# Performance work log

Measured on AMD Instinct MI355X. Metric: run time of the kernel, lower is better.

## Reference

```python
import jax, jax.numpy as jnp
import numpy as np

N_NODES = 100000
HIDDEN = 64
N_EDGES = 1600000


def _sage_conv(x, edge_index, Wl, Wr, b):
    # PyG SAGEConv (mean aggr): out_i = W_l @ mean_{j->i} x_j + W_r @ x_i + b
    src, dst = edge_index[0], edge_index[1]
    msg = x[src]                                      # [E, H] gather
    agg = jax.ops.segment_sum(msg, dst, num_segments=N_NODES)  # [N, H]
    deg = jax.ops.segment_sum(jnp.ones((msg.shape[0],), x.dtype), dst,
                              num_segments=N_NODES)
    agg = agg / jnp.maximum(deg, 1.0)[:, None]
    return agg @ Wl.T + x @ Wr.T + b


def setup_inputs() -> dict:
    key = jax.random.key(0)
    ks = jax.random.split(key, 8)
    s = 1.0 / np.sqrt(HIDDEN)
    return {
        "emb": jax.random.normal(ks[0], (N_NODES, HIDDEN), jnp.float32),
        "Wl1": jax.random.normal(ks[1], (HIDDEN, HIDDEN), jnp.float32) * s,
        "Wr1": jax.random.normal(ks[2], (HIDDEN, HIDDEN), jnp.float32) * s,
        "b1": jnp.zeros((HIDDEN,), jnp.float32),
        "Wl2": jax.random.normal(ks[3], (HIDDEN, HIDDEN), jnp.float32) * s,
        "Wr2": jax.random.normal(ks[4], (HIDDEN, HIDDEN), jnp.float32) * s,
        "b2": jnp.zeros((HIDDEN,), jnp.float32),
        "node_id": jnp.arange(N_NODES, dtype=jnp.int64 if jax.config.jax_enable_x64 else jnp.int32),
        "edge_index": jax.random.randint(ks[5], (2, N_EDGES), 0, N_NODES),
    }


def reference(emb, Wl1, Wr1, b1, Wl2, Wr2, b2, node_id, edge_index):
    # Embedding lookup
    x = emb[node_id]                                   # [N, H]
    # GNN: relu(conv1) -> conv2
    x = jax.nn.relu(_sage_conv(x, edge_index, Wl1, Wr1, b1))
    x = _sage_conv(x, edge_index, Wl2, Wr2, b2)
    # Classifier: per-edge dot product of endpoint features
    ef1 = x[edge_index[0]]                             # [E, H]
    ef2 = x[edge_index[1]]                             # [E, H]
    return (ef1 * ef2).sum(axis=-1)                    # [E]
```

## Files before the change

### kernel.cpp

```cpp
#include <hip/hip_runtime.h>

#define N_NODES 100000
#define HID 64
#define N_EDGES 1600000
#define NB 391
#define NBP 392
#define NHB 256
#define C_EPB 6400
#define GATHER_BLOCKS 6250

typedef __attribute__((ext_vector_type(8))) short bf16x8;
typedef __attribute__((ext_vector_type(4))) float f32x4;

__device__ __forceinline__ unsigned short f2bf(float f) {
    unsigned u = __float_as_uint(f);
    u = (u + 0x7FFFu + ((u >> 16) & 1u)) >> 16;
    return (unsigned short)u;
}
__device__ __forceinline__ float bf2f(unsigned short h) {
    return __uint_as_float(((unsigned)h) << 16);
}
__device__ __forceinline__ float bflo(unsigned w) { return __uint_as_float(w << 16); }
__device__ __forceinline__ float bfhi(unsigned w) { return __uint_as_float(w & 0xFFFF0000u); }

__global__ void gather_hist_kernel(const float* __restrict__ emb,
                                   const int* __restrict__ nid,
                                   unsigned short* __restrict__ xh,
                                   const int* __restrict__ dst,
                                   int* __restrict__ bhist_part) {
    if (blockIdx.x < GATHER_BLOCKS) {
        int i = blockIdx.x * blockDim.x + threadIdx.x;
        const int total = N_NODES * (HID / 4);
        if (i >= total) return;
        int row = i >> 4;
        int c   = i & 15;
        int s   = nid[row];
        float4 v = reinterpret_cast<const float4*>(emb)[(size_t)s * 16 + c];
        uint2 p;
        p.x = (unsigned)f2bf(v.x) | ((unsigned)f2bf(v.y) << 16);
        p.y = (unsigned)f2bf(v.z) | ((unsigned)f2bf(v.w) << 16);
        reinterpret_cast<uint2*>(xh)[(size_t)row * 16 + c] = p;
        return;
    }
    __shared__ int h[NB];
    for (int i = threadIdx.x; i < NB; i += blockDim.x) h[i] = 0;
    __syncthreads();
    int hb = blockIdx.x - GATHER_BLOCKS;
    const int nt = NHB * 256;
    const int4* d4 = (const int4*)dst;
    for (int q = hb * blockDim.x + threadIdx.x; q < N_EDGES / 4; q += nt) {
        int4 v = d4[q];
        atomicAdd(&h[v.x >> 8], 1);
        atomicAdd(&h[v.y >> 8], 1);
        atomicAdd(&h[v.z >> 8], 1);
        atomicAdd(&h[v.w >> 8], 1);
    }
    __syncthreads();
    for (int i = threadIdx.x; i < NB; i += blockDim.x)
        bhist_part[hb * NBP + i] = h[i];
}

__global__ void bucket_scan(const int* __restrict__ bhist_part,
                            int* __restrict__ boff,
                            int* __restrict__ bcursor) {
    __shared__ int s[512];
    int v = 0;
    if (threadIdx.x < NB) {
        #pragma unroll 8
        for (int p = 0; p < NHB; ++p) v += bhist_part[p * NBP + threadIdx.x];
    }
    s[threadIdx.x] = v;
    __syncthreads();
    for (int off = 1; off < 512; off <<= 1) {
        int t = (threadIdx.x >= off) ? s[threadIdx.x - off] : 0;
        __syncthreads();
        s[threadIdx.x] += t;
        __syncthreads();
    }
    if (threadIdx.x < NB) {
        int ex = s[threadIdx.x] - v;
        boff[threadIdx.x] = ex;
        bcursor[threadIdx.x] = ex;
    }
}

__global__ void bucket_scatter(const int* __restrict__ src,
                               const int* __restrict__ dst,
                               int* __restrict__ bcursor,
                               int2* __restrict__ pairs) {
    __shared__ int h[NB];
    __shared__ int base[NB];
    for (int i = threadIdx.x; i < NB; i += blockDim.x) h[i] = 0;
    __syncthreads();
    int e0 = blockIdx.x * C_EPB;
    int e1 = e0 + C_EPB; if (e1 > N_EDGES) e1 = N_EDGES;
    for (int e = e0 + threadIdx.x; e < e1; e += blockDim.x)
        atomicAdd(&h[dst[e] >> 8], 1);
    __syncthreads();
    for (int i = threadIdx.x; i < NB; i += blockDim.x) {
        int c = h[i];
        base[i] = c ? atomicAdd(&bcursor[i], c) : 0;
    }
    __syncthreads();
    for (int i = threadIdx.x; i < NB; i += blockDim.x) h[i] = 0;
    __syncthreads();
    for (int e = e0 + threadIdx.x; e < e1; e += blockDim.x) {
        int d = dst[e];
        int b = d >> 8;
        int slot = base[b] + atomicAdd(&h[b], 1);
        pairs[slot] = make_int2(src[e], d);
    }
}

__global__ void bucket_csr(const int2* __restrict__ pairs,
                           const int* __restrict__ boff,
                           const int* __restrict__ bcursor,
                           int* __restrict__ row_start,
                           int* __restrict__ adj) {
    __shared__ int cnt[256];
    __shared__ int sc[256];
    int b = blockIdx.x;
    int node0 = b << 8;
    int p0 = boff[b];
    int p1 = bcursor[b];
    int t = threadIdx.x;
    cnt[t] = 0;
    __syncthreads();
    for (int p = p0 + t; p < p1; p += 256)
        atomicAdd(&cnt[pairs[p].y & 255], 1);
    __syncthreads();
    int v = cnt[t];
    sc[t] = v;
    __syncthreads();
    for (int off = 1; off < 256; off <<= 1) {
        int u = (t >= off) ? sc[t - off] : 0;
        __syncthreads();
        sc[t] += u;
        __syncthreads();
    }
    sc[t] = p0 + sc[t] - v;
    __syncthreads();
    int node = node0 + t;
    if (node <= N_NODES) row_start[node] = sc[t];
    __syncthreads();
    for (int p = p0 + t; p < p1; p += 256) {
        int2 pr = pairs[p];
        int slot = atomicAdd(&sc[pr.y & 255], 1);
        adj[slot] = pr.x;
    }
}

__global__ void agg_kernel(const int* __restrict__ row_start,
                           const int* __restrict__ adj,
                           const unsigned short* __restrict__ xh,
                           unsigned short* __restrict__ M) {
    int lane = threadIdx.x & 63;
    int g = lane >> 3;
    int c = lane & 7;
    int wpb = blockDim.x >> 6;
    int wid = blockIdx.x * wpb + (threadIdx.x >> 6);
    int stride = gridDim.x * wpb;
    const uint4* xw = (const uint4*)xh;
    uint4* Mw = (uint4*)M;
    const int NQ = N_NODES / 8;
    for (int q = wid; q < NQ; q += stride) {
        int row = q * 8 + g;
        int beg = row_start[row], end = row_start[row + 1];
        float a0 = 0.f, a1 = 0.f, a2 = 0.f, a3 = 0.f;
        float a4 = 0.f, a5 = 0.f, a6 = 0.f, a7 = 0.f;
        int j = beg;
        for (; j + 7 < end; j += 8) {
            int s0 = adj[j],     s1 = adj[j + 1], s2 = adj[j + 2], s3 = adj[j + 3];
            int s4 = adj[j + 4], s5 = adj[j + 5], s6 = adj[j + 6], s7 = adj[j + 7];
            uint4 v0 = xw[(size_t)s0 * 8 + c];
            uint4 v1 = xw[(size_t)s1 * 8 + c];
            uint4 v2 = xw[(size_t)s2 * 8 + c];
            uint4 v3 = xw[(size_t)s3 * 8 + c];
            uint4 v4 = xw[(size_t)s4 * 8 + c];
            uint4 v5 = xw[(size_t)s5 * 8 + c];
            uint4 v6 = xw[(size_t)s6 * 8 + c];
            uint4 v7 = xw[(size_t)s7 * 8 + c];
            a0 += bflo(v0.x) + bflo(v1.x) + bflo(v2.x) + bflo(v3.x)
                + bflo(v4.x) + bflo(v5.x) + bflo(v6.x) + bflo(v7.x);
            a1 += bfhi(v0.x) + bfhi(v1.x) + bfhi(v2.x) + bfhi(v3.x)
                + bfhi(v4.x) + bfhi(v5.x) + bfhi(v6.x) + bfhi(v7.x);
            a2 += bflo(v0.y) + bflo(v1.y) + bflo(v2.y) + bflo(v3.y)
                + bflo(v4.y) + bflo(v5.y) + bflo(v6.y) + bflo(v7.y);
            a3 += bfhi(v0.y) + bfhi(v1.y) + bfhi(v2.y) + bfhi(v3.y)
                + bfhi(v4.y) + bfhi(v5.y) + bfhi(v6.y) + bfhi(v7.y);
            a4 += bflo(v0.z) + bflo(v1.z) + bflo(v2.z) + bflo(v3.z)
                + bflo(v4.z) + bflo(v5.z) + bflo(v6.z) + bflo(v7.z);
            a5 += bfhi(v0.z) + bfhi(v1.z) + bfhi(v2.z) + bfhi(v3.z)
                + bfhi(v4.z) + bfhi(v5.z) + bfhi(v6.z) + bfhi(v7.z);
            a6 += bflo(v0.w) + bflo(v1.w) + bflo(v2.w) + bflo(v3.w)
                + bflo(v4.w) + bflo(v5.w) + bflo(v6.w) + bflo(v7.w);
            a7 += bfhi(v0.w) + bfhi(v1.w) + bfhi(v2.w) + bfhi(v3.w)
                + bfhi(v4.w) + bfhi(v5.w) + bfhi(v6.w) + bfhi(v7.w);
        }
        if (j + 3 < end) {
            int s0 = adj[j], s1 = adj[j + 1], s2 = adj[j + 2], s3 = adj[j + 3];
            uint4 v0 = xw[(size_t)s0 * 8 + c];
            uint4 v1 = xw[(size_t)s1 * 8 + c];
            uint4 v2 = xw[(size_t)s2 * 8 + c];
            uint4 v3 = xw[(size_t)s3 * 8 + c];
            a0 += bflo(v0.x) + bflo(v1.x) + bflo(v2.x) + bflo(v3.x);
            a1 += bfhi(v0.x) + bfhi(v1.x) + bfhi(v2.x) + bfhi(v3.x);
            a2 += bflo(v0.y) + bflo(v1.y) + bflo(v2.y) + bflo(v3.y);
            a3 += bfhi(v0.y) + bfhi(v1.y) + bfhi(v2.y) + bfhi(v3.y);
            a4 += bflo(v0.z) + bflo(v1.z) + bflo(v2.z) + bflo(v3.z);
            a5 += bfhi(v0.z) + bfhi(v1.z) + bfhi(v2.z) + bfhi(v3.z);
            a6 += bflo(v0.w) + bflo(v1.w) + bflo(v2.w) + bflo(v3.w);
            a7 += bfhi(v0.w) + bfhi(v1.w) + bfhi(v2.w) + bfhi(v3.w);
            j += 4;
        }
        for (; j < end; ++j) {
            uint4 v = xw[(size_t)adj[j] * 8 + c];
            a0 += bflo(v.x); a1 += bfhi(v.x);
            a2 += bflo(v.y); a3 += bfhi(v.y);
            a4 += bflo(v.z); a5 += bfhi(v.z);
            a6 += bflo(v.w); a7 += bfhi(v.w);
        }
        float inv = 1.0f / fmaxf((float)(end - beg), 1.0f);
        uint4 p;
        p.x = (unsigned)f2bf(a0 * inv) | ((unsigned)f2bf(a1 * inv) << 16);
        p.y = (unsigned)f2bf(a2 * inv) | ((unsigned)f2bf(a3 * inv) << 16);
        p.z = (unsigned)f2bf(a4 * inv) | ((unsigned)f2bf(a5 * inv) << 16);
        p.w = (unsigned)f2bf(a6 * inv) | ((unsigned)f2bf(a7 * inv) << 16);
        Mw[(size_t)row * 8 + c] = p;
    }
}

__global__ void gemm_kernel(const unsigned short* __restrict__ Am,
                            const unsigned short* __restrict__ As,
                            const float* __restrict__ Wl,
                            const float* __restrict__ Wr,
                            const float* __restrict__ bias,
                            unsigned short* __restrict__ H,
                            int relu) {
    int lane = threadIdx.x & 63;
    int m = lane & 15, quad = lane >> 4;

    bf16x8 wf[2][2][4];
    for (int mat = 0; mat < 2; ++mat) {
        const float* W = mat ? Wr : Wl;
        for (int ks = 0; ks < 2; ++ks)
            for (int ct = 0; ct < 4; ++ct) {
                const float* p = W + (ct * 16 + m) * HID + ks * 32 + quad * 8;
                bf16x8 f;
                #pragma unroll
                for (int j = 0; j < 8; ++j) f[j] = (short)f2bf(p[j]);
                wf[mat][ks][ct] = f;
            }
    }
    float bv[4];
    #pragma unroll
    for (int ct = 0; ct < 4; ++ct) bv[ct] = bias[ct * 16 + m];

    int wpb = blockDim.x >> 6;
    int wid = blockIdx.x * wpb + (threadIdx.x >> 6);
    int stride = gridDim.x * wpb;
    const int NT = N_NODES / 16;
    for (int t = wid; t < NT; t += stride) {
        f32x4 acc[4] = {{0,0,0,0},{0,0,0,0},{0,0,0,0},{0,0,0,0}};
        size_t rowbase = ((size_t)t * 16 + m) * HID;
        #pragma unroll
        for (int ks = 0; ks < 2; ++ks) {
            bf16x8 a0 = *(const bf16x8*)(Am + rowbase + ks * 32 + quad * 8);
            bf16x8 a1 = *(const bf16x8*)(As + rowbase + ks * 32 + quad * 8);
            #pragma unroll
            for (int ct = 0; ct < 4; ++ct) {
                acc[ct] = __builtin_amdgcn_mfma_f32_16x16x32_bf16(a0, wf[0][ks][ct], acc[ct], 0, 0, 0);
                acc[ct] = __builtin_amdgcn_mfma_f32_16x16x32_bf16(a1, wf[1][ks][ct], acc[ct], 0, 0, 0);
            }
        }
        #pragma unroll
        for (int ct = 0; ct < 4; ++ct) {
            #pragma unroll
            for (int r = 0; r < 4; ++r) {
                float v = acc[ct][r] + bv[ct];
                if (relu) v = fmaxf(v, 0.f);
                H[((size_t)t * 16 + quad * 4 + r) * HID + ct * 16 + m] = f2bf(v);
            }
        }
    }
}

__global__ void edge_dot_kernel(const int* __restrict__ src,
                                const int* __restrict__ dst,
                                const unsigned short* __restrict__ h,
                                float* __restrict__ out) {
    int t = blockIdx.x * blockDim.x + threadIdx.x;
    int g = t >> 3;
    int c = t & 7;
    int e0 = g * 2;
    if (e0 >= N_EDGES) return;
    int a0 = src[e0],     b0 = dst[e0];
    int a1 = src[e0 + 1], b1 = dst[e0 + 1];
    const uint4* h4 = reinterpret_cast<const uint4*>(h);
    uint4 va0 = h4[(size_t)a0 * 8 + c];
    uint4 vb0 = h4[(size_t)b0 * 8 + c];
    uint4 va1 = h4[(size_t)a1 * 8 + c];
    uint4 vb1 = h4[(size_t)b1 * 8 + c];
    float p0 = bflo(va0.x) * bflo(vb0.x) + bfhi(va0.x) * bfhi(vb0.x)
             + bflo(va0.y) * bflo(vb0.y) + bfhi(va0.y) * bfhi(vb0.y)
             + bflo(va0.z) * bflo(vb0.z) + bfhi(va0.z) * bfhi(vb0.z)
             + bflo(va0.w) * bflo(vb0.w) + bfhi(va0.w) * bfhi(vb0.w);
    float p1 = bflo(va1.x) * bflo(vb1.x) + bfhi(va1.x) * bfhi(vb1.x)
             + bflo(va1.y) * bflo(vb1.y) + bfhi(va1.y) * bfhi(vb1.y)
             + bflo(va1.z) * bflo(vb1.z) + bfhi(va1.z) * bfhi(vb1.z)
             + bflo(va1.w) * bflo(vb1.w) + bfhi(va1.w) * bfhi(vb1.w);
    p0 += __shfl_xor(p0, 1); p0 += __shfl_xor(p0, 2); p0 += __shfl_xor(p0, 4);
    p1 += __shfl_xor(p1, 1); p1 += __shfl_xor(p1, 2); p1 += __shfl_xor(p1, 4);
    if (c == 0) reinterpret_cast<float2*>(out)[g] = make_float2(p0, p1);
}

extern "C" void kernel_launch(void* const* d_in, const int* in_sizes, int n_in,
                              void* d_out, int out_size, void* d_ws, size_t ws_size,
                              hipStream_t stream) {
    const float* emb = (const float*)d_in[0];
    const float* Wl1 = (const float*)d_in[1];
    const float* Wr1 = (const float*)d_in[2];
    const float* b1  = (const float*)d_in[3];
    const float* Wl2 = (const float*)d_in[4];
    const float* Wr2 = (const float*)d_in[5];
    const float* b2  = (const float*)d_in[6];
    const int*   nid = (const int*)d_in[7];
    const int*   ei  = (const int*)d_in[8];
    const int* esrc = ei;
    const int* edst = ei + N_EDGES;
    float* out = (float*)d_out;

    const size_t NH = (size_t)N_NODES * HID;
    unsigned short* xh  = (unsigned short*)d_ws;
    unsigned short* h1h = xh + NH;
    unsigned short* h2h = h1h + NH;
    unsigned short* M   = h2h + NH;
    int* ib        = (int*)(M + NH);
    int* row_start = ib;
    int* adj       = ib + N_NODES + 64;
    int2* pairs    = (int2*)(adj + N_EDGES + 64);
    int* bhist_part = (int*)(pairs + N_EDGES);
    int* boff      = bhist_part + NHB * NBP;
    int* bcursor   = boff + NB + 1;

    gather_hist_kernel<<<GATHER_BLOCKS + NHB, 256, 0, stream>>>(emb, nid, xh, edst, bhist_part);

    bucket_scan<<<1, 512, 0, stream>>>(bhist_part, boff, bcursor);
    bucket_scatter<<<(N_EDGES + C_EPB - 1) / C_EPB, 256, 0, stream>>>(esrc, edst, bcursor, pairs);
    bucket_csr<<<NB, 256, 0, stream>>>(pairs, boff, bcursor, row_start, adj);

    agg_kernel<<<2048, 256, 0, stream>>>(row_start, adj, xh, M);
    gemm_kernel<<<512, 256, 0, stream>>>(M, xh, Wl1, Wr1, b1, h1h, 1);

    agg_kernel<<<2048, 256, 0, stream>>>(row_start, adj, h1h, M);
    gemm_kernel<<<512, 256, 0, stream>>>(M, h1h, Wl2, Wr2, b2, h2h, 0);

    edge_dot_kernel<<<((size_t)(N_EDGES / 2) * 8 + 255) / 256, 256, 0, stream>>>(esrc, edst, h2h, out);
}
```

Measured before the change: 279.1 us.

## Fuse mean aggregation with MFMA projection and prepack bf16 weights in prep kernel

```diff
diff --git a/kernel.cpp b/kernel.cpp
--- a/kernel.cpp
+++ b/kernel.cpp
@@ -17,17 +17,19 @@
     u = (u + 0x7FFFu + ((u >> 16) & 1u)) >> 16;
     return (unsigned short)u;
 }
-__device__ __forceinline__ float bf2f(unsigned short h) {
-    return __uint_as_float(((unsigned)h) << 16);
-}
 __device__ __forceinline__ float bflo(unsigned w) { return __uint_as_float(w << 16); }
 __device__ __forceinline__ float bfhi(unsigned w) { return __uint_as_float(w & 0xFFFF0000u); }
 
-__global__ void gather_hist_kernel(const float* __restrict__ emb,
-                                   const int* __restrict__ nid,
-                                   unsigned short* __restrict__ xh,
-                                   const int* __restrict__ dst,
-                                   int* __restrict__ bhist_part) {
+__global__ void prep_kernel(const float* __restrict__ emb,
+                            const int* __restrict__ nid,
+                            unsigned short* __restrict__ xh,
+                            const int* __restrict__ dst,
+                            int* __restrict__ bhist_part,
+                            const float* __restrict__ Wl1,
+                            const float* __restrict__ Wr1,
+                            const float* __restrict__ Wl2,
+                            const float* __restrict__ Wr2,
+                            unsigned short* __restrict__ wpack) {
     if (blockIdx.x < GATHER_BLOCKS) {
         int i = blockIdx.x * blockDim.x + threadIdx.x;
         const int total = N_NODES * (HID / 4);
@@ -42,22 +44,40 @@
         reinterpret_cast<uint2*>(xh)[(size_t)row * 16 + c] = p;
         return;
     }
-    __shared__ int h[NB];
-    for (int i = threadIdx.x; i < NB; i += blockDim.x) h[i] = 0;
-    __syncthreads();
-    int hb = blockIdx.x - GATHER_BLOCKS;
-    const int nt = NHB * 256;
-    const int4* d4 = (const int4*)dst;
-    for (int q = hb * blockDim.x + threadIdx.x; q < N_EDGES / 4; q += nt) {
-        int4 v = d4[q];
-        atomicAdd(&h[v.x >> 8], 1);
-        atomicAdd(&h[v.y >> 8], 1);
-        atomicAdd(&h[v.z >> 8], 1);
-        atomicAdd(&h[v.w >> 8], 1);
-    }
-    __syncthreads();
-    for (int i = threadIdx.x; i < NB; i += blockDim.x)
-        bhist_part[hb * NBP + i] = h[i];
+    if (blockIdx.x < GATHER_BLOCKS + NHB) {
+        __shared__ int h[NB];
+        for (int i = threadIdx.x; i < NB; i += blockDim.x) h[i] = 0;
+        __syncthreads();
+        int hb = blockIdx.x - GATHER_BLOCKS;
+        const int nt = NHB * 256;
+        const int4* d4 = (const int4*)dst;
+        for (int q = hb * blockDim.x + threadIdx.x; q < N_EDGES / 4; q += nt) {
+            int4 v = d4[q];
+            atomicAdd(&h[v.x >> 8], 1);
+            atomicAdd(&h[v.y >> 8], 1);
+            atomicAdd(&h[v.z >> 8], 1);
+            atomicAdd(&h[v.w >> 8], 1);
+        }
+        __syncthreads();
+        for (int i = threadIdx.x; i < NB; i += blockDim.x)
+            bhist_part[hb * NBP + i] = h[i];
+        return;
+    }
+    int L = blockIdx.x - GATHER_BLOCKS - NHB;
+    const float* WL = L ? Wl2 : Wl1;
+    const float* WR = L ? Wr2 : Wr1;
+    for (int idx = threadIdx.x; idx < 1024; idx += 256) {
+        int lane = idx & 63;
+        int ct   = (idx >> 6) & 3;
+        int ks   = (idx >> 8) & 1;
+        int mat  = idx >> 9;
+        const float* W = mat ? WR : WL;
+        int m = lane & 15, quad = lane >> 4;
+        const float* p = W + (ct * 16 + m) * HID + ks * 32 + quad * 8;
+        unsigned short* q = wpack + ((size_t)L * 1024 + idx) * 8;
+        #pragma unroll
+        for (int j = 0; j < 8; ++j) q[j] = f2bf(p[j]);
+    }
 }
 
 __global__ void bucket_scan(const int* __restrict__ bhist_part,
@@ -150,127 +170,93 @@
     }
 }
 
-__global__ void agg_kernel(const int* __restrict__ row_start,
-                           const int* __restrict__ adj,
-                           const unsigned short* __restrict__ xh,
-                           unsigned short* __restrict__ M) {
+__global__ void sage_fused_kernel(const int* __restrict__ row_start,
+                                  const int* __restrict__ adj,
+                                  const unsigned short* __restrict__ X,
+                                  const unsigned short* __restrict__ wpack,
+                                  const float* __restrict__ bias,
+                                  unsigned short* __restrict__ H,
+                                  int relu) {
     int lane = threadIdx.x & 63;
-    int g = lane >> 3;
-    int c = lane & 7;
-    int wpb = blockDim.x >> 6;
-    int wid = blockIdx.x * wpb + (threadIdx.x >> 6);
-    int stride = gridDim.x * wpb;
-    const uint4* xw = (const uint4*)xh;
-    uint4* Mw = (uint4*)M;
-    const int NQ = N_NODES / 8;
-    for (int q = wid; q < NQ; q += stride) {
-        int row = q * 8 + g;
-        int beg = row_start[row], end = row_start[row + 1];
-        float a0 = 0.f, a1 = 0.f, a2 = 0.f, a3 = 0.f;
-        float a4 = 0.f, a5 = 0.f, a6 = 0.f, a7 = 0.f;
-        int j = beg;
-        for (; j + 7 < end; j += 8) {
-            int s0 = adj[j],     s1 = adj[j + 1], s2 = adj[j + 2], s3 = adj[j + 3];
-            int s4 = adj[j + 4], s5 = adj[j + 5], s6 = adj[j + 6], s7 = adj[j + 7];
-            uint4 v0 = xw[(size_t)s0 * 8 + c];
-            uint4 v1 = xw[(size_t)s1 * 8 + c];
-            uint4 v2 = xw[(size_t)s2 * 8 + c];
-            uint4 v3 = xw[(size_t)s3 * 8 + c];
-            uint4 v4 = xw[(size_t)s4 * 8 + c];
-            uint4 v5 = xw[(size_t)s5 * 8 + c];
-            uint4 v6 = xw[(size_t)s6 * 8 + c];
-            uint4 v7 = xw[(size_t)s7 * 8 + c];
-            a0 += bflo(v0.x) + bflo(v1.x) + bflo(v2.x) + bflo(v3.x)
-                + bflo(v4.x) + bflo(v5.x) + bflo(v6.x) + bflo(v7.x);
-            a1 += bfhi(v0.x) + bfhi(v1.x) + bfhi(v2.x) + bfhi(v3.x)
-                + bfhi(v4.x) + bfhi(v5.x) + bfhi(v6.x) + bfhi(v7.x);
-            a2 += bflo(v0.y) + bflo(v1.y) + bflo(v2.y) + bflo(v3.y)
-                + bflo(v4.y) + bflo(v5.y) + bflo(v6.y) + bflo(v7.y);
-            a3 += bfhi(v0.y) + bfhi(v1.y) + bfhi(v2.y) + bfhi(v3.y)
-                + bfhi(v4.y) + bfhi(v5.y) + bfhi(v6.y) + bfhi(v7.y);
-            a4 += bflo(v0.z) + bflo(v1.z) + bflo(v2.z) + bflo(v3.z)
-                + bflo(v4.z) + bflo(v5.z) + bflo(v6.z) + bflo(v7.z);
-            a5 += bfhi(v0.z) + bfhi(v1.z) + bfhi(v2.z) + bfhi(v3.z)
-                + bfhi(v4.z) + bfhi(v5.z) + bfhi(v6.z) + bfhi(v7.z);
-            a6 += bflo(v0.w) + bflo(v1.w) + bflo(v2.w) + bflo(v3.w)
-                + bflo(v4.w) + bflo(v5.w) + bflo(v6.w) + bflo(v7.w);
-            a7 += bfhi(v0.w) + bfhi(v1.w) + bfhi(v2.w) + bfhi(v3.w)
-                + bfhi(v4.w) + bfhi(v5.w) + bfhi(v6.w) + bfhi(v7.w);
-        }
-        if (j + 3 < end) {
-            int s0 = adj[j], s1 = adj[j + 1], s2 = adj[j + 2], s3 = adj[j + 3];
-            uint4 v0 = xw[(size_t)s0 * 8 + c];
-            uint4 v1 = xw[(size_t)s1 * 8 + c];
-            uint4 v2 = xw[(size_t)s2 * 8 + c];
-            uint4 v3 = xw[(size_t)s3 * 8 + c];
-            a0 += bflo(v0.x) + bflo(v1.x) + bflo(v2.x) + bflo(v3.x);
-            a1 += bfhi(v0.x) + bfhi(v1.x) + bfhi(v2.x) + bfhi(v3.x);
-            a2 += bflo(v0.y) + bflo(v1.y) + bflo(v2.y) + bflo(v3.y);
-            a3 += bfhi(v0.y) + bfhi(v1.y) + bfhi(v2.y) + bfhi(v3.y);
-            a4 += bflo(v0.z) + bflo(v1.z) + bflo(v2.z) + bflo(v3.z);
-            a5 += bfhi(v0.z) + bfhi(v1.z) + bfhi(v2.z) + bfhi(v3.z);
-            a6 += bflo(v0.w) + bflo(v1.w) + bflo(v2.w) + bflo(v3.w);
-            a7 += bfhi(v0.w) + bfhi(v1.w) + bfhi(v2.w) + bfhi(v3.w);
-            j += 4;
-        }
-        for (; j < end; ++j) {
-            uint4 v = xw[(size_t)adj[j] * 8 + c];
-            a0 += bflo(v.x); a1 += bfhi(v.x);
-            a2 += bflo(v.y); a3 += bfhi(v.y);
-            a4 += bflo(v.z); a5 += bfhi(v.z);
-            a6 += bflo(v.w); a7 += bfhi(v.w);
-        }
-        float inv = 1.0f / fmaxf((float)(end - beg), 1.0f);
-        uint4 p;
-        p.x = (unsigned)f2bf(a0 * inv) | ((unsigned)f2bf(a1 * inv) << 16);
-        p.y = (unsigned)f2bf(a2 * inv) | ((unsigned)f2bf(a3 * inv) << 16);
-        p.z = (unsigned)f2bf(a4 * inv) | ((unsigned)f2bf(a5 * inv) << 16);
-        p.w = (unsigned)f2bf(a6 * inv) | ((unsigned)f2bf(a7 * inv) << 16);
-        Mw[(size_t)row * 8 + c] = p;
-    }
-}
-
-__global__ void gemm_kernel(const unsigned short* __restrict__ Am,
-                            const unsigned short* __restrict__ As,
-                            const float* __restrict__ Wl,
-                            const float* __restrict__ Wr,
-                            const float* __restrict__ bias,
-                            unsigned short* __restrict__ H,
-                            int relu) {
-    int lane = threadIdx.x & 63;
-    int m = lane & 15, quad = lane >> 4;
-
-    bf16x8 wf[2][2][4];
-    for (int mat = 0; mat < 2; ++mat) {
-        const float* W = mat ? Wr : Wl;
-        for (int ks = 0; ks < 2; ++ks)
-            for (int ct = 0; ct < 4; ++ct) {
-                const float* p = W + (ct * 16 + m) * HID + ks * 32 + quad * 8;
-                bf16x8 f;
-                #pragma unroll
-                for (int j = 0; j < 8; ++j) f[j] = (short)f2bf(p[j]);
-                wf[mat][ks][ct] = f;
-            }
-    }
-    float bv[4];
-    #pragma unroll
-    for (int ct = 0; ct < 4; ++ct) bv[ct] = bias[ct * 16 + m];
-
+    int m    = lane & 15;
+    int quad = lane >> 4;
     int wpb = blockDim.x >> 6;
     int wid = blockIdx.x * wpb + (threadIdx.x >> 6);
     int stride = gridDim.x * wpb;
     const int NT = N_NODES / 16;
+    const uint4* xw = (const uint4*)X;
+    const bf16x8* wp = (const bf16x8*)wpack;
+    float bv[4];
+    #pragma unroll
+    for (int ct = 0; ct < 4; ++ct) bv[ct] = bias[ct * 16 + m];
+
     for (int t = wid; t < NT; t += stride) {
+        int row = t * 16 + m;
+        int beg = row_start[row], end = row_start[row + 1];
+        float a0 = 0.f, a1 = 0.f, a2 = 0.f, a3 = 0.f;
+        float a4 = 0.f, a5 = 0.f, a6 = 0.f, a7 = 0.f;
+        float b0 = 0.f, b1 = 0.f, b2 = 0.f, b3 = 0.f;
+        float b4 = 0.f, b5 = 0.f, b6 = 0.f, b7 = 0.f;
+        int j = beg;
+        for (; j + 3 < end; j += 4) {
+            int s0 = adj[j], s1 = adj[j + 1], s2 = adj[j + 2], s3 = adj[j + 3];
+            uint4 u0 = xw[(size_t)s0 * 8 + quad];
+            uint4 v0 = xw[(size_t)s0 * 8 + 4 + quad];
+            uint4 u1 = xw[(size_t)s1 * 8 + quad];
+            uint4 v1 = xw[(size_t)s1 * 8 + 4 + quad];
+            uint4 u2 = xw[(size_t)s2 * 8 + quad];
+            uint4 v2 = xw[(size_t)s2 * 8 + 4 + quad];
+            uint4 u3 = xw[(size_t)s3 * 8 + quad];
+            uint4 v3 = xw[(size_t)s3 * 8 + 4 + quad];
+            a0 += bflo(u0.x) + bflo(u1.x) + bflo(u2.x) + bflo(u3.x);
+            a1 += bfhi(u0.x) + bfhi(u1.x) + bfhi(u2.x) + bfhi(u3.x);
+            a2 += bflo(u0.y) + bflo(u1.y) + bflo(u2.y) + bflo(u3.y);
+            a3 += bfhi(u0.y) + bfhi(u1.y) + bfhi(u2.y) + bfhi(u3.y);
+            a4 += bflo(u0.z) + bflo(u1.z) + bflo(u2.z) + bflo(u3.z);
+            a5 += bfhi(u0.z) + bfhi(u1.z) + bfhi(u2.z) + bfhi(u3.z);
+            a6 += bflo(u0.w) + bflo(u1.w) + bflo(u2.w) + bflo(u3.w);
+            a7 += bfhi(u0.w) + bfhi(u1.w) + bfhi(u2.w) + bfhi(u3.w);
+            b0 += bflo(v0.x) + bflo(v1.x) + bflo(v2.x) + bflo(v3.x);
+            b1 += bfhi(v0.x) + bfhi(v1.x) + bfhi(v2.x) + bfhi(v3.x);
+            b2 += bflo(v0.y) + bflo(v1.y) + bflo(v2.y) + bflo(v3.y);
+            b3 += bfhi(v0.y) + bfhi(v1.y) + bfhi(v2.y) + bfhi(v3.y);
+            b4 += bflo(v0.z) + bflo(v1.z) + bflo(v2.z) + bflo(v3.z);
+            b5 += bfhi(v0.z) + bfhi(v1.z) + bfhi(v2.z) + bfhi(v3.z);
+            b6 += bflo(v0.w) + bflo(v1.w) + bflo(v2.w) + bflo(v3.w);
+            b7 += bfhi(v0.w) + bfhi(v1.w) + bfhi(v2.w) + bfhi(v3.w);
+        }
+        for (; j < end; ++j) {
+            int s = adj[j];
+            uint4 u = xw[(size_t)s * 8 + quad];
+            uint4 v = xw[(size_t)s * 8 + 4 + quad];
+            a0 += bflo(u.x); a1 += bfhi(u.x); a2 += bflo(u.y); a3 += bfhi(u.y);
+            a4 += bflo(u.z); a5 += bfhi(u.z); a6 += bflo(u.w); a7 += bfhi(u.w);
+            b0 += bflo(v.x); b1 += bfhi(v.x); b2 += bflo(v.y); b3 += bfhi(v.y);
+            b4 += bflo(v.z); b5 += bfhi(v.z); b6 += bflo(v.w); b7 += bfhi(v.w);
+        }
+        float inv = 1.0f / fmaxf((float)(end - beg), 1.0f);
+        bf16x8 am0, am1;
+        am0[0] = (short)f2bf(a0 * inv); am0[1] = (short)f2bf(a1 * inv);
+        am0[2] = (short)f2bf(a2 * inv); am0[3] = (short)f2bf(a3 * inv);
+        am0[4] = (short)f2bf(a4 * inv); am0[5] = (short)f2bf(a5 * inv);
+        am0[6] = (short)f2bf(a6 * inv); am0[7] = (short)f2bf(a7 * inv);
+        am1[0] = (short)f2bf(b0 * inv); am1[1] = (short)f2bf(b1 * inv);
+        am1[2] = (short)f2bf(b2 * inv); am1[3] = (short)f2bf(b3 * inv);
+        am1[4] = (short)f2bf(b4 * inv); am1[5] = (short)f2bf(b5 * inv);
+        am1[6] = (short)f2bf(b6 * inv); am1[7] = (short)f2bf(b7 * inv);
+        bf16x8 as0 = *(const bf16x8*)(X + (size_t)row * HID + quad * 8);
+        bf16x8 as1 = *(const bf16x8*)(X + (size_t)row * HID + 32 + quad * 8);
         f32x4 acc[4] = {{0,0,0,0},{0,0,0,0},{0,0,0,0},{0,0,0,0}};
-        size_t rowbase = ((size_t)t * 16 + m) * HID;
         #pragma unroll
         for (int ks = 0; ks < 2; ++ks) {
-            bf16x8 a0 = *(const bf16x8*)(Am + rowbase + ks * 32 + quad * 8);
-            bf16x8 a1 = *(const bf16x8*)(As + rowbase + ks * 32 + quad * 8);
+            bf16x8 amean = ks ? am1 : am0;
+            bf16x8 aself = ks ? as1 : as0;
             #pragma unroll
             for (int ct = 0; ct < 4; ++ct) {
-                acc[ct] = __builtin_amdgcn_mfma_f32_16x16x32_bf16(a0, wf[0][ks][ct], acc[ct], 0, 0, 0);
-                acc[ct] = __builtin_amdgcn_mfma_f32_16x16x32_bf16(a1, wf[1][ks][ct], acc[ct], 0, 0, 0);
+                acc[ct] = __builtin_amdgcn_mfma_f32_16x16x32_bf16(
+                    amean, wp[(size_t)ks * 256 + ct * 64 + lane], acc[ct], 0, 0, 0);
+                acc[ct] = __builtin_amdgcn_mfma_f32_16x16x32_bf16(
+                    aself, wp[(size_t)512 + ks * 256 + ct * 64 + lane], acc[ct], 0, 0, 0);
             }
         }
         #pragma unroll
@@ -334,26 +320,26 @@
     unsigned short* xh  = (unsigned short*)d_ws;
     unsigned short* h1h = xh + NH;
     unsigned short* h2h = h1h + NH;
-    unsigned short* M   = h2h + NH;
-    int* ib        = (int*)(M + NH);
+    int* ib        = (int*)(h2h + NH);
     int* row_start = ib;
     int* adj       = ib + N_NODES + 64;
     int2* pairs    = (int2*)(adj + N_EDGES + 64);
     int* bhist_part = (int*)(pairs + N_EDGES);
     int* boff      = bhist_part + NHB * NBP;
     int* bcursor   = boff + NB + 1;
-
-    gather_hist_kernel<<<GATHER_BLOCKS + NHB, 256, 0, stream>>>(emb, nid, xh, edst, bhist_part);
+    unsigned short* wpack = (unsigned short*)(bcursor + NB + 1);
+
+    prep_kernel<<<GATHER_BLOCKS + NHB + 2, 256, 0, stream>>>(
+        emb, nid, xh, edst, bhist_part, Wl1, Wr1, Wl2, Wr2, wpack);
 
     bucket_scan<<<1, 512, 0, stream>>>(bhist_part, boff, bcursor);
     bucket_scatter<<<(N_EDGES + C_EPB - 1) / C_EPB, 256, 0, stream>>>(esrc, edst, bcursor, pairs);
     bucket_csr<<<NB, 256, 0, stream>>>(pairs, boff, bcursor, row_start, adj);
 
-    agg_kernel<<<2048, 256, 0, stream>>>(row_start, adj, xh, M);
-    gemm_kernel<<<512, 256, 0, stream>>>(M, xh, Wl1, Wr1, b1, h1h, 1);
-
-    agg_kernel<<<2048, 256, 0, stream>>>(row_start, adj, h1h, M);
-    gemm_kernel<<<512, 256, 0, stream>>>(M, h1h, Wl2, Wr2, b2, h2h, 0);
+    sage_fused_kernel<<<1563, 256, 0, stream>>>(row_start, adj, xh,
+                                                wpack, b1, h1h, 1);
+    sage_fused_kernel<<<1563, 256, 0, stream>>>(row_start, adj, h1h,
+                                                wpack + 1024 * 8, b2, h2h, 0);
 
     edge_dot_kernel<<<((size_t)(N_EDGES / 2) * 8 + 255) / 256, 256, 0, stream>>>(esrc, edst, h2h, out);
 }
```

Result: slower. 290.1 us (+3.9%).

## Replace two-level bucket sort CSR build with per-node degree count, scan, atomic scatter

Applied to the files above, without the earlier changes.

```diff
diff --git a/kernel.cpp b/kernel.cpp
--- a/kernel.cpp
+++ b/kernel.cpp
@@ -3,11 +3,9 @@
 #define N_NODES 100000
 #define HID 64
 #define N_EDGES 1600000
-#define NB 391
-#define NBP 392
 #define NHB 256
-#define C_EPB 6400
 #define GATHER_BLOCKS 6250
+#define SCAN_NPT 98
 
 typedef __attribute__((ext_vector_type(8))) short bf16x8;
 typedef __attribute__((ext_vector_type(4))) float f32x4;
@@ -17,17 +15,14 @@
     u = (u + 0x7FFFu + ((u >> 16) & 1u)) >> 16;
     return (unsigned short)u;
 }
-__device__ __forceinline__ float bf2f(unsigned short h) {
-    return __uint_as_float(((unsigned)h) << 16);
-}
 __device__ __forceinline__ float bflo(unsigned w) { return __uint_as_float(w << 16); }
 __device__ __forceinline__ float bfhi(unsigned w) { return __uint_as_float(w & 0xFFFF0000u); }
 
-__global__ void gather_hist_kernel(const float* __restrict__ emb,
-                                   const int* __restrict__ nid,
-                                   unsigned short* __restrict__ xh,
-                                   const int* __restrict__ dst,
-                                   int* __restrict__ bhist_part) {
+__global__ void prep_kernel(const float* __restrict__ emb,
+                            const int* __restrict__ nid,
+                            unsigned short* __restrict__ xh,
+                            const int* __restrict__ dst,
+                            int* __restrict__ deg) {
     if (blockIdx.x < GATHER_BLOCKS) {
         int i = blockIdx.x * blockDim.x + threadIdx.x;
         const int total = N_NODES * (HID / 4);
@@ -42,112 +37,56 @@
         reinterpret_cast<uint2*>(xh)[(size_t)row * 16 + c] = p;
         return;
     }
-    __shared__ int h[NB];
-    for (int i = threadIdx.x; i < NB; i += blockDim.x) h[i] = 0;
-    __syncthreads();
     int hb = blockIdx.x - GATHER_BLOCKS;
     const int nt = NHB * 256;
     const int4* d4 = (const int4*)dst;
     for (int q = hb * blockDim.x + threadIdx.x; q < N_EDGES / 4; q += nt) {
         int4 v = d4[q];
-        atomicAdd(&h[v.x >> 8], 1);
-        atomicAdd(&h[v.y >> 8], 1);
-        atomicAdd(&h[v.z >> 8], 1);
-        atomicAdd(&h[v.w >> 8], 1);
-    }
+        atomicAdd(&deg[v.x], 1);
+        atomicAdd(&deg[v.y], 1);
+        atomicAdd(&deg[v.z], 1);
+        atomicAdd(&deg[v.w], 1);
+    }
+}
+
+__global__ void scan_kernel(const int* __restrict__ deg,
+                            int* __restrict__ row_start,
+                            int* __restrict__ cursor) {
+    __shared__ int part[1024];
+    int t = threadIdx.x;
+    int i0 = t * SCAN_NPT;
+    int i1 = i0 + SCAN_NPT; if (i1 > N_NODES) i1 = N_NODES;
+    int s = 0;
+    for (int i = i0; i < i1; ++i) s += deg[i];
+    part[t] = s;
     __syncthreads();
-    for (int i = threadIdx.x; i < NB; i += blockDim.x)
-        bhist_part[hb * NBP + i] = h[i];
-}
-
-__global__ void bucket_scan(const int* __restrict__ bhist_part,
-                            int* __restrict__ boff,
-                            int* __restrict__ bcursor) {
-    __shared__ int s[512];
-    int v = 0;
-    if (threadIdx.x < NB) {
-        #pragma unroll 8
-        for (int p = 0; p < NHB; ++p) v += bhist_part[p * NBP + threadIdx.x];
-    }
-    s[threadIdx.x] = v;
-    __syncthreads();
-    for (int off = 1; off < 512; off <<= 1) {
-        int t = (threadIdx.x >= off) ? s[threadIdx.x - off] : 0;
+    for (int off = 1; off < 1024; off <<= 1) {
+        int u = (t >= off) ? part[t - off] : 0;
         __syncthreads();
-        s[threadIdx.x] += t;
+        part[t] += u;
         __syncthreads();
     }
-    if (threadIdx.x < NB) {
-        int ex = s[threadIdx.x] - v;
-        boff[threadIdx.x] = ex;
-        bcursor[threadIdx.x] = ex;
-    }
-}
-
-__global__ void bucket_scatter(const int* __restrict__ src,
+    int running = part[t] - s;
+    for (int i = i0; i < i1; ++i) {
+        row_start[i] = running;
+        cursor[i]    = running;
+        running += deg[i];
+    }
+    if (t == 0) row_start[N_NODES] = N_EDGES;
+}
+
+__global__ void scatter_kernel(const int* __restrict__ src,
                                const int* __restrict__ dst,
-                               int* __restrict__ bcursor,
-                               int2* __restrict__ pairs) {
-    __shared__ int h[NB];
-    __shared__ int base[NB];
-    for (int i = threadIdx.x; i < NB; i += blockDim.x) h[i] = 0;
-    __syncthreads();
-    int e0 = blockIdx.x * C_EPB;
-    int e1 = e0 + C_EPB; if (e1 > N_EDGES) e1 = N_EDGES;
-    for (int e = e0 + threadIdx.x; e < e1; e += blockDim.x)
-        atomicAdd(&h[dst[e] >> 8], 1);
-    __syncthreads();
-    for (int i = threadIdx.x; i < NB; i += blockDim.x) {
-        int c = h[i];
-        base[i] = c ? atomicAdd(&bcursor[i], c) : 0;
-    }
-    __syncthreads();
-    for (int i = threadIdx.x; i < NB; i += blockDim.x) h[i] = 0;
-    __syncthreads();
-    for (int e = e0 + threadIdx.x; e < e1; e += blockDim.x) {
-        int d = dst[e];
-        int b = d >> 8;
-        int slot = base[b] + atomicAdd(&h[b], 1);
-        pairs[slot] = make_int2(src[e], d);
-    }
-}
-
-__global__ void bucket_csr(const int2* __restrict__ pairs,
-                           const int* __restrict__ boff,
-                           const int* __restrict__ bcursor,
-                           int* __restrict__ row_start,
-                           int* __restrict__ adj) {
-    __shared__ int cnt[256];
-    __shared__ int sc[256];
-    int b = blockIdx.x;
-    int node0 = b << 8;
-    int p0 = boff[b];
-    int p1 = bcursor[b];
-    int t = threadIdx.x;
-    cnt[t] = 0;
-    __syncthreads();
-    for (int p = p0 + t; p < p1; p += 256)
-        atomicAdd(&cnt[pairs[p].y & 255], 1);
-    __syncthreads();
-    int v = cnt[t];
-    sc[t] = v;
-    __syncthreads();
-    for (int off = 1; off < 256; off <<= 1) {
-        int u = (t >= off) ? sc[t - off] : 0;
-        __syncthreads();
-        sc[t] += u;
-        __syncthreads();
-    }
-    sc[t] = p0 + sc[t] - v;
-    __syncthreads();
-    int node = node0 + t;
-    if (node <= N_NODES) row_start[node] = sc[t];
-    __syncthreads();
-    for (int p = p0 + t; p < p1; p += 256) {
-        int2 pr = pairs[p];
-        int slot = atomicAdd(&sc[pr.y & 255], 1);
-        adj[slot] = pr.x;
-    }
+                               int* __restrict__ cursor,
+                               int* __restrict__ adj) {
+    int q = blockIdx.x * blockDim.x + threadIdx.x;
+    if (q >= N_EDGES / 4) return;
+    int4 s = reinterpret_cast<const int4*>(src)[q];
+    int4 d = reinterpret_cast<const int4*>(dst)[q];
+    adj[atomicAdd(&cursor[d.x], 1)] = s.x;
+    adj[atomicAdd(&cursor[d.y], 1)] = s.y;
+    adj[atomicAdd(&cursor[d.z], 1)] = s.z;
+    adj[atomicAdd(&cursor[d.w], 1)] = s.w;
 }
 
 __global__ void agg_kernel(const int* __restrict__ row_start,
@@ -338,16 +277,15 @@
     int* ib        = (int*)(M + NH);
     int* row_start = ib;
     int* adj       = ib + N_NODES + 64;
-    int2* pairs    = (int2*)(adj + N_EDGES + 64);
-    int* bhist_part = (int*)(pairs + N_EDGES);
-    int* boff      = bhist_part + NHB * NBP;
-    int* bcursor   = boff + NB + 1;
-
-    gather_hist_kernel<<<GATHER_BLOCKS + NHB, 256, 0, stream>>>(emb, nid, xh, edst, bhist_part);
-
-    bucket_scan<<<1, 512, 0, stream>>>(bhist_part, boff, bcursor);
-    bucket_scatter<<<(N_EDGES + C_EPB - 1) / C_EPB, 256, 0, stream>>>(esrc, edst, bcursor, pairs);
-    bucket_csr<<<NB, 256, 0, stream>>>(pairs, boff, bcursor, row_start, adj);
+    int* deg       = adj + N_EDGES + 64;
+    int* cursor    = deg + N_NODES;
+
+    hipMemsetAsync(deg, 0, N_NODES * sizeof(int), stream);
+
+    prep_kernel<<<GATHER_BLOCKS + NHB, 256, 0, stream>>>(emb, nid, xh, edst, deg);
+
+    scan_kernel<<<1, 1024, 0, stream>>>(deg, row_start, cursor);
+    scatter_kernel<<<(N_EDGES / 4 + 255) / 256, 256, 0, stream>>>(esrc, edst, cursor, adj);
 
     agg_kernel<<<2048, 256, 0, stream>>>(row_start, adj, xh, M);
     gemm_kernel<<<512, 256, 0, stream>>>(M, xh, Wl1, Wr1, b1, h1h, 1);
```

After: 654.4 us. 2.34x slower.
